# Kernel optimization log

Hardware: AMD Instinct MI355X
Metric: run time of the kernel (lower is better)

## Reference

```python
import jax, jax.numpy as jnp
import numpy as np

B, T, N, L, D, H = 8, 6, 24, 1024, 512, 8
DH = D // H
EPS = 1e-5


def setup_inputs() -> dict:
    key = jax.random.key(0)
    ks = jax.random.split(key, 8)
    q = jax.random.normal(ks[0], (B, T, N, D), jnp.float32)
    k = jax.random.normal(ks[1], (B, T, L, D), jnp.float32)
    v = jax.random.normal(ks[2], (B, T, L, D), jnp.float32)
    attn_mask = jax.random.randint(ks[3], (T * N, T * L), 0, 10) == 0
    s = D ** -0.5
    Wq = jax.random.normal(ks[4], (D, D), jnp.float32) * s
    Wk = jax.random.normal(ks[5], (D, D), jnp.float32) * s
    Wv = jax.random.normal(ks[6], (D, D), jnp.float32) * s
    Wo = jax.random.normal(ks[7], (D, D), jnp.float32) * s
    return {"q": q, "k": k, "v": v, "attn_mask": attn_mask,
            "Wq": Wq, "Wk": Wk, "Wv": Wv, "Wo": Wo}


def reference(q, k, v, attn_mask, Wq, Wk, Wv, Wo):
    # Projections (torch Linear: y = x @ W.T), split into heads
    qp = (q.reshape(B, T * N, D) @ Wq.T).reshape(B, T * N, H, DH).transpose(0, 2, 1, 3)
    kp = (k.reshape(B, T * L, D) @ Wk.T).reshape(B, T * L, H, DH).transpose(0, 2, 1, 3)
    vp = (v.reshape(B, T * L, D) @ Wv.T).reshape(B, T * L, H, DH).transpose(0, 2, 1, 3)
    qp = qp * (DH ** -0.5)
    # scores: [B, H, T*N, T*L]
    scores = jnp.einsum('bhnd,bhmd->bhnm', qp, kp)
    scores = jnp.where(attn_mask[None, None], -jnp.inf, scores)
    # cross-head softmax: normalize over the combined (H*N) axis per (b, t, tl)
    a = scores.reshape(B, H, T, N, T * L).transpose(0, 2, 4, 1, 3)  # B,T,TL,H,N
    a = a.reshape(B, T, T * L, H * N)
    a = jax.nn.softmax(a, axis=-1)
    a = a.reshape(B, T, T * L, H, N).transpose(0, 3, 1, 4, 2).reshape(B, H, T * N, T * L)
    a = jnp.where(attn_mask[None, None], 0.0, a)
    attn_vis = a
    # renormalize along key axis
    a = a / (a.sum(axis=-1, keepdims=True) + EPS)
    out = jnp.einsum('bhnm,bhmd->bhnd', a, vp)  # B,H,T*N,DH
    out = out.transpose(0, 2, 1, 3).reshape(B, T * N, D)
    out = (out @ Wo.T).reshape(B, T, N, D)
    return out, attn_vis
```

## Files before the change

### kernel.cpp

```cpp
#include <hip/hip_runtime.h>
#include <hip/hip_bf16.h>
#include <math.h>

#define CB 8
#define CT 6
#define CN 24
#define CL 1024
#define CD 512
#define CH 8
#define CDH 64
#define CTN 144
#define CTL 6144
#define CMS 16
#define CEPS 1e-5f

typedef __bf16 bf16x8 __attribute__((ext_vector_type(8)));
typedef float  f32x4  __attribute__((ext_vector_type(4)));

#define MFMA16(a,b,c) __builtin_amdgcn_mfma_f32_16x16x32_bf16(a,b,c,0,0,0)

union BF8 { unsigned short s[8]; bf16x8 v; };

static __device__ __forceinline__ unsigned short f2bf(float x){
    union { float f; unsigned u; } c; c.f = x;
    return (unsigned short)((c.u + 0x7FFFu + ((c.u >> 16) & 1u)) >> 16);
}

static __device__ __forceinline__ float bf2f(unsigned short u){
    union { unsigned u; float f; } c; c.u = ((unsigned)u) << 16;
    return c.f;
}

static __device__ __forceinline__ bf16x8 pack8(f32x4 a, f32x4 b){
    BF8 r;
    r.s[0]=f2bf(a[0]); r.s[1]=f2bf(a[1]); r.s[2]=f2bf(a[2]); r.s[3]=f2bf(a[3]);
    r.s[4]=f2bf(b[0]); r.s[5]=f2bf(b[1]); r.s[6]=f2bf(b[2]); r.s[7]=f2bf(b[3]);
    return r.v;
}

static __device__ __forceinline__ bf16x8 ldbf8(const unsigned short* __restrict__ p){
    return *(const bf16x8*)p;
}

#define GL16(gp, lp) __builtin_amdgcn_global_load_lds((const unsigned int*)(gp), (unsigned int*)(lp), 16, 0, 0)

__global__ void cvt_w_kernel(const float* __restrict__ w0, const float* __restrict__ w1,
                             const float* __restrict__ w2, const float* __restrict__ w3,
                             unsigned short* __restrict__ o0, unsigned short* __restrict__ o1,
                             unsigned short* __restrict__ o2, unsigned short* __restrict__ o3){
    int i = blockIdx.x*blockDim.x + threadIdx.x;
    const int n = CD*CD;
    if      (i < n)   o0[i]       = f2bf(w0[i]);
    else if (i < 2*n) o1[i-n]     = f2bf(w1[i-n]);
    else if (i < 3*n) o2[i-2*n]   = f2bf(w2[i-2*n]);
    else if (i < 4*n) o3[i-3*n]   = f2bf(w3[i-3*n]);
}

__global__ void maskb_kernel(const int* __restrict__ mask, unsigned int* __restrict__ maskb){
    int i = blockIdx.x*blockDim.x + threadIdx.x;
    if (i >= CT*CTL) return;
    int t = i / CTL, m = i - t*CTL;
    unsigned w = 0;
    for (int n = 0; n < 24; ++n)
        if (mask[(size_t)(t*24 + n)*CTL + m] != 0) w |= (1u << n);
    maskb[i] = w;
}

template<int MODE>
__global__ __launch_bounds__(512, 3) void proj_bg(
    const float* __restrict__ X, const unsigned short* __restrict__ W,
    unsigned short* __restrict__ out)
{
    __shared__ union {
        unsigned short As[8192];
        float epi[32][129];
    } sm;

    int nwg = gridDim.x*gridDim.y;
    int id  = blockIdx.y*gridDim.x + blockIdx.x;
    int q8 = nwg >> 3, r8 = nwg & 7;
    int xcd = id & 7, rk = id >> 3;
    int swz = (xcd < r8 ? xcd*(q8+1) : r8*(q8+1) + (xcd-r8)*q8) + rk;
    int ctile = swz & 3;
    int bt    = swz >> 2;

    int tid = threadIdx.x;
    int lane = tid & 63, wave = tid >> 6;
    int wr = wave >> 2, wc = wave & 3;
    int qq = lane & 15, g = lane >> 4;

    const float* gaf = X + (size_t)(bt*128 + wave*16 + qq)*CD + g*8;
    const unsigned short* gbw = W + (size_t)(ctile*128 + wc*32 + qq)*CD + g*8;

    f32x4 acc[4][2] = {};

    for (int k0 = 0; k0 < CD; k0 += 64) {
        #pragma unroll
        for (int x = 0; x < 2; ++x) {
            f32x4 a0 = *(const f32x4*)(gaf + k0 + x*32);
            f32x4 a1 = *(const f32x4*)(gaf + k0 + x*32 + 4);
            *(bf16x8*)(sm.As + wave*1024 + x*512 + lane*8) = pack8(a0, a1);
        }
        __syncthreads();
        #pragma unroll
        for (int x = 0; x < 2; ++x) {
            bf16x8 af[4];
            #pragma unroll
            for (int mf = 0; mf < 4; ++mf)
                af[mf] = *(const bf16x8*)&sm.As[((wr*4 + mf)*2 + x)*512 + lane*8];
            #pragma unroll
            for (int nf = 0; nf < 2; ++nf) {
                bf16x8 bw = ldbf8(gbw + (size_t)(nf*16)*CD + k0 + x*32);
                #pragma unroll
                for (int mf = 0; mf < 4; ++mf)
                    acc[mf][nf] = MFMA16(af[mf], bw, acc[mf][nf]);
            }
        }
        __syncthreads();
    }

    for (int p = 0; p < 4; ++p) {
        if (wr == (p >> 1)) {
            #pragma unroll
            for (int mh = 0; mh < 2; ++mh) {
                int mf = (p&1)*2 + mh;
                #pragma unroll
                for (int nf = 0; nf < 2; ++nf)
                    #pragma unroll
                    for (int r = 0; r < 4; ++r)
                        sm.epi[mh*16 + 4*g + r][wc*32 + nf*16 + qq] = acc[mf][nf][r];
            }
        }
        __syncthreads();
        if (MODE == 1) {
            #pragma unroll
            for (int i = 0; i < 8; ++i) {
                int c2 = i*16 + wave*2 + (lane>>5);
                int gr = bt*128 + p*32 + (lane & 31);
                int bb = gr / CTL, pos = gr - bb*CTL;
                int hh = ctile*2 + (c2>>6), dh = c2 & 63;
                out[((size_t)(bb*CH + hh)*64 + dh)*CTL + pos] = f2bf(sm.epi[lane&31][c2]);
            }
        } else {
            #pragma unroll
            for (int i = 0; i < 8; ++i) {
                int task = i*8 + wave;
                int lr = task >> 1, ch = task & 1;
                float val = sm.epi[lr][ch*64 + lane];
                int gr = bt*128 + p*32 + lr;
                int bb = gr / CTL, pos = gr - bb*CTL;
                int hh = ctile*2 + ch;
                out[((size_t)(bb*CH + hh)*CTL + pos)*64 + lane] = f2bf(val);
            }
        }
        __syncthreads();
    }
}

template<int MODE, int AFMT>
__global__ __launch_bounds__(512, 4) void gemm_m97(
    const void* __restrict__ Ap, const unsigned short* __restrict__ W,
    void* __restrict__ outv, int posPer, int rowoff, float scale)
{
    __shared__ union {
        struct { unsigned short As[8192]; unsigned short Bs[8192]; } s;
        float epi[32][129];
    } sm;

    int nwg = gridDim.x*gridDim.y;
    int id  = blockIdx.y*gridDim.x + blockIdx.x;
    int q8 = nwg >> 3, r8 = nwg & 7;
    int xcd = id & 7, rk = id >> 3;
    int swz = (xcd < r8 ? xcd*(q8+1) : r8*(q8+1) + (xcd-r8)*q8) + rk;
    int ctile = swz & 3;
    int bt    = swz >> 2;

    int tid = threadIdx.x;
    int lane = tid & 63, wave = tid >> 6;
    int wr = wave >> 2, wc = wave & 3;
    int qq = lane & 15, g = lane >> 4;

    const unsigned short* gah = (const unsigned short*)Ap + (size_t)(bt*128 + wave*16 + qq)*CD + g*8;
    const unsigned short* gb  = W + (size_t)(ctile*128 + wave*16 + qq)*CD + g*8;
    const float*          gaf = (const float*)Ap + (size_t)(bt*128 + wave*16 + qq)*CD + g*8;
    unsigned short* lA = sm.s.As + wave*1024;
    unsigned short* lB = sm.s.Bs + wave*1024;

    f32x4 acc[4][2] = {};

    for (int k0 = 0; k0 < CD; k0 += 64) {
        if (AFMT == 0) {
            #pragma unroll
            for (int x = 0; x < 2; ++x) {
                f32x4 a0 = *(const f32x4*)(gaf + k0 + x*32);
                f32x4 a1 = *(const f32x4*)(gaf + k0 + x*32 + 4);
                *(bf16x8*)(sm.s.As + wave*1024 + x*512 + lane*8) = pack8(a0, a1);
            }
        } else {
            GL16(gah + k0,      lA);
            GL16(gah + k0 + 32, lA + 512);
        }
        GL16(gb + k0,      lB);
        GL16(gb + k0 + 32, lB + 512);
        __syncthreads();
        #pragma unroll
        for (int x = 0; x < 2; ++x) {
            bf16x8 af[4], bf[2];
            #pragma unroll
            for (int mf = 0; mf < 4; ++mf)
                af[mf] = *(const bf16x8*)&sm.s.As[((wr*4 + mf)*2 + x)*512 + lane*8];
            #pragma unroll
            for (int nf = 0; nf < 2; ++nf)
                bf[nf] = *(const bf16x8*)&sm.s.Bs[((wc*2 + nf)*2 + x)*512 + lane*8];
            #pragma unroll
            for (int mf = 0; mf < 4; ++mf)
                #pragma unroll
                for (int nf = 0; nf < 2; ++nf)
                    acc[mf][nf] = MFMA16(af[mf], bf[nf], acc[mf][nf]);
        }
        __syncthreads();
    }

    unsigned short* outu = (unsigned short*)outv;
    float* outf = (float*)outv;
    for (int p = 0; p < 4; ++p) {
        if (wr == (p >> 1)) {
            #pragma unroll
            for (int mh = 0; mh < 2; ++mh) {
                int mf = (p&1)*2 + mh;
                #pragma unroll
                for (int nf = 0; nf < 2; ++nf)
                    #pragma unroll
                    for (int r = 0; r < 4; ++r)
                        sm.epi[mh*16 + 4*g + r][wc*32 + nf*16 + qq] = acc[mf][nf][r]*scale;
            }
        }
        __syncthreads();
        #pragma unroll
        for (int i = 0; i < 8; ++i) {
            int task = i*8 + wave;
            int lr = task >> 1, ch = task & 1;
            float val = sm.epi[lr][ch*64 + lane];
            int gr = rowoff + bt*128 + p*32 + lr;
            if (MODE == 2) {
                outf[(size_t)gr*CD + ctile*128 + ch*64 + lane] = val;
            } else {
                int bb = gr / posPer, pos = gr - bb*posPer;
                int hh = ctile*2 + ch;
                outu[((size_t)(bb*CH + hh)*posPer + pos)*64 + lane] = f2bf(val);
            }
        }
        __syncthreads();
    }
}

__global__ __launch_bounds__(256) void scores_a_kernel(
    const unsigned short* __restrict__ qp, const unsigned short* __restrict__ kp,
    const unsigned int* __restrict__ maskb,
    float* __restrict__ pmax, float* __restrict__ psum)
{
    __shared__ float S[CTN][65];
    int mt = blockIdx.x;
    int h = blockIdx.y, b = blockIdx.z;
    int lane = threadIdx.x & 63, wave = threadIdx.x >> 6;
    const unsigned short* qbase = qp + (size_t)(b*CH + h)*CTN*64;
    const unsigned short* kbase = kp + (size_t)(b*CH + h)*CTL*64;
    int koff = 8*(lane>>4);
    f32x4 acc[3][4] = {};
    for (int k0 = 0; k0 < 64; k0 += 32) {
        bf16x8 bfr[4];
        #pragma unroll
        for (int cf = 0; cf < 4; ++cf)
            bfr[cf] = ldbf8(kbase + (size_t)(mt*64 + cf*16 + (lane&15))*64 + k0 + koff);
        #pragma unroll
        for (int i = 0; i < 3; ++i) {
            int rt = wave + 4*i;
            if (rt < 9) {
                bf16x8 a = ldbf8(qbase + (size_t)(rt*16 + (lane&15))*64 + k0 + koff);
                #pragma unroll
                for (int cf = 0; cf < 4; ++cf)
                    acc[i][cf] = MFMA16(a, bfr[cf], acc[i][cf]);
            }
        }
    }
    #pragma unroll
    for (int i = 0; i < 3; ++i) {
        int rt = wave + 4*i;
        if (rt < 9) {
            #pragma unroll
            for (int cf = 0; cf < 4; ++cf)
                #pragma unroll
                for (int r = 0; r < 4; ++r)
                    S[rt*16 + 4*(lane>>4) + r][cf*16 + (lane&15)] = acc[i][cf][r];
        }
    }
    __syncthreads();
    int mg0 = mt*64;
    for (int task = threadIdx.x; task < CT*64; task += 256) {
        int t = task >> 6, ml = task & 63;
        int mg = mg0 + ml;
        unsigned w = maskb[(size_t)t*CTL + mg];
        float mx = -INFINITY;
        float sv[24];
        #pragma unroll
        for (int i = 0; i < 24; ++i) {
            float s = ((w >> i) & 1u) ? -INFINITY : S[t*24 + i][ml];
            sv[i] = s;
            mx = fmaxf(mx, s);
        }
        float sum = 0.f;
        if (mx > -INFINITY) {
            #pragma unroll
            for (int i = 0; i < 24; ++i)
                if (sv[i] > -INFINITY) sum += __expf(sv[i] - mx);
        }
        size_t idx = ((size_t)(b*CH + h)*CT + t)*CTL + mg;
        pmax[idx] = mx; psum[idx] = sum;
    }
}

__global__ void combine_kernel(const float* __restrict__ pmax, const float* __restrict__ psum,
                               const unsigned int* __restrict__ maskb,
                               float2* __restrict__ stat2){
    size_t i = (size_t)blockIdx.x*blockDim.x + threadIdx.x;
    if (i >= (size_t)CB*CT*CTL) return;
    int m = (int)(i % CTL);
    size_t bt = i / CTL;
    int t = (int)(bt % CT), b = (int)(bt / CT);
    float pm[CH], ps[CH];
    float mx = -INFINITY;
    #pragma unroll
    for (int h = 0; h < CH; ++h) {
        size_t idx = ((size_t)(b*CH + h)*CT + t)*CTL + m;
        pm[h] = pmax[idx]; ps[h] = psum[idx];
        mx = fmaxf(mx, pm[h]);
    }
    float s = 0.f;
    if (mx > -INFINITY) {
        #pragma unroll
        for (int h = 0; h < CH; ++h)
            if (pm[h] > -INFINITY) s += ps[h]*__expf(pm[h] - mx);
    }
    float lse = (mx > -INFINITY && s > 0.f) ? mx + __logf(s) : 0.f;
    float2 o; o.x = lse; o.y = __uint_as_float(maskb[(size_t)t*CTL + m]);
    stat2[i] = o;
}

__global__ __launch_bounds__(64, 3) void fused_bpv(
    const unsigned short* __restrict__ qp, const unsigned short* __restrict__ kp,
    const unsigned short* __restrict__ vpT,
    const float2* __restrict__ stat2,
    float* __restrict__ avis, unsigned short* __restrict__ pvpart,
    float* __restrict__ rowpart)
{
    __shared__ unsigned short abf[16][68];
    __shared__ float av32[16][65];

    int ms = blockIdx.x;
    int ry = blockIdx.y;
    int bh = blockIdx.z;
    int b = bh >> 3;
    int lane = threadIdx.x;
    int qq = lane & 15, g = lane >> 4;
    int koff = 8*g;
    int nrt = (ry < 4) ? 2 : 1;
    int rt0 = ry*2;

    const unsigned short* qbase = qp + (size_t)bh*CTN*64;
    const unsigned short* kbase = kp + (size_t)bh*CTL*64;
    const unsigned short* vb    = vpT + (size_t)bh*64*CTL;

    int rbit[2];
    const float2* stp[2];
    float* avbase[2];
    bf16x8 qf[2][2];
    #pragma unroll
    for (int i = 0; i < 2; ++i) {
        int rt = rt0 + i;
        if (i >= nrt) rt = rt0;
        int qrow = rt*16 + qq;
        int t = qrow / 24;
        rbit[i] = qrow - t*24;
        stp[i] = stat2 + (size_t)(b*CT + t)*CTL;
        avbase[i] = avis + ((size_t)bh*CTN + rt*16)*CTL;
        #pragma unroll
        for (int x = 0; x < 2; ++x)
            qf[i][x] = ldbf8(qbase + (size_t)qrow*64 + x*32 + koff);
    }

    f32x4 pv[2][4] = {};
    float rs[2] = {0.f, 0.f};

    for (int mt = 0; mt < 6; ++mt) {
        int mg0 = ms*384 + mt*64;
        bf16x8 vf[2][4];
        #pragma unroll
        for (int x = 0; x < 2; ++x)
            #pragma unroll
            for (int cf = 0; cf < 4; ++cf)
                vf[x][cf] = ldbf8(vb + (size_t)(cf*16 + qq)*CTL + mg0 + x*32 + koff);
        f32x4 sacc[2][4] = {};
        #pragma unroll
        for (int x = 0; x < 2; ++x) {
            bf16x8 kf[4];
            #pragma unroll
            for (int cf = 0; cf < 4; ++cf)
                kf[cf] = ldbf8(kbase + (size_t)(mg0 + cf*16 + qq)*64 + x*32 + koff);
            #pragma unroll
            for (int cf = 0; cf < 4; ++cf)
                sacc[0][cf] = MFMA16(kf[cf], qf[0][x], sacc[0][cf]);
            if (nrt == 2) {
                #pragma unroll
                for (int cf = 0; cf < 4; ++cf)
                    sacc[1][cf] = MFMA16(kf[cf], qf[1][x], sacc[1][cf]);
            }
        }
        #pragma unroll
        for (int i = 0; i < 2; ++i) {
            if (i < nrt) {
                #pragma unroll
                for (int cf = 0; cf < 4; ++cf) {
                    const f32x4* sp = (const f32x4*)(stp[i] + mg0 + cf*16 + 4*g);
                    f32x4 s0 = sp[0], s1 = sp[1];
                    f32x4 av;
                    av[0] = ((__float_as_uint(s0[1]) >> rbit[i]) & 1u) ? 0.f : __expf(sacc[i][cf][0] - s0[0]);
                    av[1] = ((__float_as_uint(s0[3]) >> rbit[i]) & 1u) ? 0.f : __expf(sacc[i][cf][1] - s0[2]);
                    av[2] = ((__float_as_uint(s1[1]) >> rbit[i]) & 1u) ? 0.f : __expf(sacc[i][cf][2] - s1[0]);
                    av[3] = ((__float_as_uint(s1[3]) >> rbit[i]) & 1u) ? 0.f : __expf(sacc[i][cf][3] - s1[2]);
                    *(f32x4*)&av32[qq][cf*16 + 4*g] = av;
                    unsigned short u4[4] = { f2bf(av[0]), f2bf(av[1]), f2bf(av[2]), f2bf(av[3]) };
                    *(unsigned long long*)&abf[qq][cf*16 + 4*g] = *(unsigned long long*)u4;
                    rs[i] += av[0] + av[1] + av[2] + av[3];
                }
                #pragma unroll
                for (int p = 0; p < 4; ++p) {
                    int row = 4*p + (lane >> 4);
                    int col = 4*(lane & 15);
                    f32x4 v4 = *(const f32x4*)&av32[row][col];
                    __builtin_nontemporal_store(v4, (f32x4*)(avbase[i] + (size_t)row*CTL + mg0 + col));
                }
                #pragma unroll
                for (int x = 0; x < 2; ++x) {
                    bf16x8 af = *(const bf16x8*)&abf[qq][x*32 + koff];
                    #pragma unroll
                    for (int cf = 0; cf < 4; ++cf)
                        pv[i][cf] = MFMA16(af, vf[x][cf], pv[i][cf]);
                }
            }
        }
    }

    #pragma unroll
    for (int i = 0; i < 2; ++i) {
        if (i < nrt) {
            int rt = rt0 + i;
            float s = rs[i];
            s += __shfl_xor(s, 16);
            s += __shfl_xor(s, 32);
            if (g == 0)
                rowpart[(size_t)ms*(CB*CH*CTN) + (size_t)bh*CTN + rt*16 + qq] = s;
            unsigned short* pb = pvpart + ((size_t)(ms*64 + bh)*CTN + rt*16)*64;
            #pragma unroll
            for (int cf = 0; cf < 4; ++cf) {
                unsigned short u4[4] = { f2bf(pv[i][cf][0]), f2bf(pv[i][cf][1]),
                                         f2bf(pv[i][cf][2]), f2bf(pv[i][cf][3]) };
                *(unsigned long long*)&pb[cf*256 + lane*4] = *(unsigned long long*)u4;
            }
        }
    }
}

__global__ void pv_reduce_kernel(const unsigned short* __restrict__ pvpart,
                                 const float* __restrict__ rowpart,
                                 unsigned short* __restrict__ oh){
    int idx = blockIdx.x*blockDim.x + threadIdx.x;
    if (idx >= CB*CH*CTN*64) return;
    int col = idx & 63;
    int rowbh = idx >> 6;
    int row = rowbh % CTN, bh = rowbh / CTN;
    float rsum = 0.f;
    #pragma unroll
    for (int ms = 0; ms < CMS; ++ms)
        rsum += rowpart[(size_t)ms*(CB*CH*CTN) + rowbh];
    int rt = row >> 4, lr = row & 15, g = lr >> 2, r = lr & 3;
    int cf = col >> 4, qq = col & 15;
    size_t off = ((size_t)bh*CTN + rt*16)*64 + cf*256 + (g*16 + qq)*4 + r;
    float s = 0.f;
    #pragma unroll
    for (int ms = 0; ms < CMS; ++ms)
        s += bf2f(pvpart[(size_t)ms*((size_t)CB*CH*CTN*64) + off]);
    float inv = 1.f / (rsum + CEPS);
    int b = bh >> 3, h = bh & 7;
    oh[((size_t)b*CTN + row)*CD + h*64 + col] = f2bf(s*inv);
}

extern "C" void kernel_launch(void* const* d_in, const int* in_sizes, int n_in,
                              void* d_out, int out_size, void* d_ws, size_t ws_size,
                              hipStream_t stream)
{
    const float* q    = (const float*)d_in[0];
    const float* k    = (const float*)d_in[1];
    const float* v    = (const float*)d_in[2];
    const int*   mask = (const int*)  d_in[3];
    const float* Wq   = (const float*)d_in[4];
    const float* Wk   = (const float*)d_in[5];
    const float* Wv   = (const float*)d_in[6];
    const float* Wo   = (const float*)d_in[7];

    float* out0 = (float*)d_out;
    float* avis = out0 + (size_t)CB*CTN*CD;

    char* p = (char*)d_ws;
    auto alloc = [&](size_t bytes) -> char* {
        char* r = p; p += (bytes + 255) & ~(size_t)255; return r;
    };
    unsigned short* Wq_bf = (unsigned short*)alloc((size_t)CD*CD*2);
    unsigned short* Wk_bf = (unsigned short*)alloc((size_t)CD*CD*2);
    unsigned short* Wv_bf = (unsigned short*)alloc((size_t)CD*CD*2);
    unsigned short* Wo_bf = (unsigned short*)alloc((size_t)CD*CD*2);
    unsigned short* qp    = (unsigned short*)alloc((size_t)CB*CH*CTN*64*2);
    unsigned short* kp    = (unsigned short*)alloc((size_t)CB*CH*CTL*64*2);
    unsigned short* vpT   = (unsigned short*)alloc((size_t)CB*CH*64*CTL*2);
    char* S = alloc((size_t)CB*CH*CT*CTL*4*2);
    float* pmax   = (float*)S;
    float* psum   = (float*)(S + (size_t)CB*CH*CT*CTL*4);
    unsigned short* pvpart = (unsigned short*)S;
    float2* stat2 = (float2*)alloc((size_t)CB*CT*CTL*8);
    unsigned int* maskb = (unsigned int*)alloc((size_t)CT*CTL*4);
    float* rowpart = (float*)alloc((size_t)CMS*CB*CH*CTN*4);
    unsigned short* oh = (unsigned short*)alloc((size_t)CB*CTN*CD*2);

    cvt_w_kernel<<<(4*CD*CD + 255)/256, 256, 0, stream>>>(Wq, Wk, Wv, Wo,
                                                          Wq_bf, Wk_bf, Wv_bf, Wo_bf);
    maskb_kernel<<<(CT*CTL + 255)/256, 256, 0, stream>>>(mask, maskb);
    gemm_m97<0,0><<<dim3(4, CB*CTN/128), 512, 0, stream>>>(q, Wq_bf, qp, CTN, 0, 0.125f);
    proj_bg<0><<<dim3(4, CB*CTL/128), 512, 0, stream>>>(k, Wk_bf, kp);
    proj_bg<1><<<dim3(4, CB*CTL/128), 512, 0, stream>>>(v, Wv_bf, vpT);
    scores_a_kernel<<<dim3(CTL/64, CH, CB), 256, 0, stream>>>(qp, kp, maskb, pmax, psum);
    combine_kernel<<<((CB*CT*CTL) + 255)/256, 256, 0, stream>>>(pmax, psum, maskb, stat2);
    fused_bpv<<<dim3(CMS, 5, CB*CH), 64, 0, stream>>>(qp, kp, vpT, stat2,
                                                      avis, pvpart, rowpart);
    pv_reduce_kernel<<<((CB*CH*CTN*64) + 255)/256, 256, 0, stream>>>(pvpart, rowpart, oh);
    gemm_m97<2,1><<<dim3(4, CB*CTN/128), 512, 0, stream>>>(oh, Wo_bf, out0, CD, 0, 1.0f);
}
```

Before: 417.9 us.

## Compute score partial softmax stats in registers with per-wave row-group blocks

The scores_a kernel drops the shared-memory score tile and the serial per-column max/sum loop. Each single-wave block now handles one pair of time slices (48 query rows) against a 64-key tile, with the MFMA operands swapped so that key positions lie along the accumulator rows. Per-column max and exp-sum are then taken with cross-lane shuffles and written as vectors. This removes the LDS round trip and the barrier and spreads the reductions over lanes, but the K tile is now loaded three times (once per row group) and each block has fewer waves.

```diff
diff --git a/kernel.cpp b/kernel.cpp
--- a/kernel.cpp
+++ b/kernel.cpp
@@ -254,68 +254,99 @@
     }
 }
 
-__global__ __launch_bounds__(256) void scores_a_kernel(
+__global__ __launch_bounds__(64, 3) void scores_a_kernel(
     const unsigned short* __restrict__ qp, const unsigned short* __restrict__ kp,
     const unsigned int* __restrict__ maskb,
     float* __restrict__ pmax, float* __restrict__ psum)
 {
-    __shared__ float S[CTN][65];
     int mt = blockIdx.x;
-    int h = blockIdx.y, b = blockIdx.z;
-    int lane = threadIdx.x & 63, wave = threadIdx.x >> 6;
-    const unsigned short* qbase = qp + (size_t)(b*CH + h)*CTN*64;
-    const unsigned short* kbase = kp + (size_t)(b*CH + h)*CTL*64;
-    int koff = 8*(lane>>4);
-    f32x4 acc[3][4] = {};
-    for (int k0 = 0; k0 < 64; k0 += 32) {
-        bf16x8 bfr[4];
+    int rg = blockIdx.y;
+    int bh = blockIdx.z;
+    int lane = threadIdx.x;
+    int qq = lane & 15, g = lane >> 4;
+    int koff = 8*g;
+    int t0 = rg*2, t1 = rg*2 + 1;
+    int mg0 = mt*64;
+
+    const unsigned short* qbase = qp + (size_t)bh*CTN*64;
+    const unsigned short* kbase = kp + (size_t)bh*CTL*64;
+
+    bf16x8 qf[3][2];
+    #pragma unroll
+    for (int i = 0; i < 3; ++i)
+        #pragma unroll
+        for (int x = 0; x < 2; ++x)
+            qf[i][x] = ldbf8(qbase + (size_t)((rg*3 + i)*16 + qq)*64 + x*32 + koff);
+
+    f32x4 sacc[3][4] = {};
+    #pragma unroll
+    for (int x = 0; x < 2; ++x) {
+        bf16x8 kf[4];
         #pragma unroll
         for (int cf = 0; cf < 4; ++cf)
-            bfr[cf] = ldbf8(kbase + (size_t)(mt*64 + cf*16 + (lane&15))*64 + k0 + koff);
-        #pragma unroll
-        for (int i = 0; i < 3; ++i) {
-            int rt = wave + 4*i;
-            if (rt < 9) {
-                bf16x8 a = ldbf8(qbase + (size_t)(rt*16 + (lane&15))*64 + k0 + koff);
-                #pragma unroll
-                for (int cf = 0; cf < 4; ++cf)
-                    acc[i][cf] = MFMA16(a, bfr[cf], acc[i][cf]);
-            }
-        }
-    }
-    #pragma unroll
-    for (int i = 0; i < 3; ++i) {
-        int rt = wave + 4*i;
-        if (rt < 9) {
+            kf[cf] = ldbf8(kbase + (size_t)(mg0 + cf*16 + qq)*64 + x*32 + koff);
+        #pragma unroll
+        for (int i = 0; i < 3; ++i)
             #pragma unroll
             for (int cf = 0; cf < 4; ++cf)
-                #pragma unroll
-                for (int r = 0; r < 4; ++r)
-                    S[rt*16 + 4*(lane>>4) + r][cf*16 + (lane&15)] = acc[i][cf][r];
-        }
-    }
-    __syncthreads();
-    int mg0 = mt*64;
-    for (int task = threadIdx.x; task < CT*64; task += 256) {
-        int t = task >> 6, ml = task & 63;
-        int mg = mg0 + ml;
-        unsigned w = maskb[(size_t)t*CTL + mg];
-        float mx = -INFINITY;
-        float sv[24];
-        #pragma unroll
-        for (int i = 0; i < 24; ++i) {
-            float s = ((w >> i) & 1u) ? -INFINITY : S[t*24 + i][ml];
-            sv[i] = s;
-            mx = fmaxf(mx, s);
-        }
-        float sum = 0.f;
-        if (mx > -INFINITY) {
-            #pragma unroll
-            for (int i = 0; i < 24; ++i)
-                if (sv[i] > -INFINITY) sum += __expf(sv[i] - mx);
-        }
-        size_t idx = ((size_t)(b*CH + h)*CT + t)*CTL + mg;
-        pmax[idx] = mx; psum[idx] = sum;
+                sacc[i][cf] = MFMA16(kf[cf], qf[i][x], sacc[i][cf]);
+    }
+
+    const unsigned int* mb0p = maskb + (size_t)t0*CTL + mg0;
+    const unsigned int* mb1p = maskb + (size_t)t1*CTL + mg0;
+    float* pm0 = pmax + ((size_t)bh*CT + t0)*CTL + mg0;
+    float* pm1 = pmax + ((size_t)bh*CT + t1)*CTL + mg0;
+    float* ps0 = psum + ((size_t)bh*CT + t0)*CTL + mg0;
+    float* ps1 = psum + ((size_t)bh*CT + t1)*CTL + mg0;
+
+    #pragma unroll
+    for (int cf = 0; cf < 4; ++cf) {
+        uint4 mb0 = *(const uint4*)(mb0p + cf*16 + 4*g);
+        uint4 mb1 = *(const uint4*)(mb1p + cf*16 + 4*g);
+        f32x4 M0, M1, E0, E1;
+        #pragma unroll
+        for (int r = 0; r < 4; ++r) {
+            unsigned w0 = (&mb0.x)[r];
+            unsigned w1 = (&mb1.x)[r];
+            float c0a = ((w0 >> qq) & 1u) ? -INFINITY : sacc[0][cf][r];
+            float s1  = sacc[1][cf][r];
+            float c0b, c1a;
+            if (qq < 8) { c0b = ((w0 >> (16 + qq)) & 1u) ? -INFINITY : s1; c1a = -INFINITY; }
+            else        { c1a = ((w1 >> (qq - 8)) & 1u) ? -INFINITY : s1; c0b = -INFINITY; }
+            float c1b = ((w1 >> (8 + qq)) & 1u) ? -INFINITY : sacc[2][cf][r];
+            float m0 = fmaxf(c0a, c0b);
+            m0 = fmaxf(m0, __shfl_xor(m0, 1));
+            m0 = fmaxf(m0, __shfl_xor(m0, 2));
+            m0 = fmaxf(m0, __shfl_xor(m0, 4));
+            m0 = fmaxf(m0, __shfl_xor(m0, 8));
+            float e0 = 0.f;
+            if (c0a > -INFINITY) e0 += __expf(c0a - m0);
+            if (c0b > -INFINITY) e0 += __expf(c0b - m0);
+            e0 += __shfl_xor(e0, 1);
+            e0 += __shfl_xor(e0, 2);
+            e0 += __shfl_xor(e0, 4);
+            e0 += __shfl_xor(e0, 8);
+            M0[r] = m0; E0[r] = e0;
+            float m1 = fmaxf(c1a, c1b);
+            m1 = fmaxf(m1, __shfl_xor(m1, 1));
+            m1 = fmaxf(m1, __shfl_xor(m1, 2));
+            m1 = fmaxf(m1, __shfl_xor(m1, 4));
+            m1 = fmaxf(m1, __shfl_xor(m1, 8));
+            float e1 = 0.f;
+            if (c1a > -INFINITY) e1 += __expf(c1a - m1);
+            if (c1b > -INFINITY) e1 += __expf(c1b - m1);
+            e1 += __shfl_xor(e1, 1);
+            e1 += __shfl_xor(e1, 2);
+            e1 += __shfl_xor(e1, 4);
+            e1 += __shfl_xor(e1, 8);
+            M1[r] = m1; E1[r] = e1;
+        }
+        if (qq == 0) {
+            *(f32x4*)(pm0 + cf*16 + 4*g) = M0;
+            *(f32x4*)(ps0 + cf*16 + 4*g) = E0;
+            *(f32x4*)(pm1 + cf*16 + 4*g) = M1;
+            *(f32x4*)(ps1 + cf*16 + 4*g) = E1;
+        }
     }
 }
 
@@ -536,7 +567,7 @@
     gemm_m97<0,0><<<dim3(4, CB*CTN/128), 512, 0, stream>>>(q, Wq_bf, qp, CTN, 0, 0.125f);
     proj_bg<0><<<dim3(4, CB*CTL/128), 512, 0, stream>>>(k, Wk_bf, kp);
     proj_bg<1><<<dim3(4, CB*CTL/128), 512, 0, stream>>>(v, Wv_bf, vpT);
-    scores_a_kernel<<<dim3(CTL/64, CH, CB), 256, 0, stream>>>(qp, kp, maskb, pmax, psum);
+    scores_a_kernel<<<dim3(CTL/64, 3, CB*CH), 64, 0, stream>>>(qp, kp, maskb, pmax, psum);
     combine_kernel<<<((CB*CT*CTL) + 255)/256, 256, 0, stream>>>(pmax, psum, maskb, stat2);
     fused_bpv<<<dim3(CMS, 5, CB*CH), 64, 0, stream>>>(qp, kp, vpT, stat2,
                                                       avis, pvpart, rowpart);
```

Result: slower. 429.8 us (+2.8%).
